# Kernel tuning notes

Measured on AMD Instinct MI355X. Metric: run time of the kernel, lower is better.

## Reference

```python
import jax, jax.numpy as jnp
import numpy as np

N_NODES = 100000
N_EDGES = 1200000
EMBED_DIM = 64
N_LAYERS = 3


def setup_inputs() -> dict:
    key = jax.random.key(0)
    k1, k2, k3, k4 = jax.random.split(key, 4)
    embeddings = jax.random.normal(k1, (N_NODES, EMBED_DIM), dtype=jnp.float32)
    edge_weight = jax.random.uniform(k2, (N_EDGES,), dtype=jnp.float32)
    edge_src = jax.random.randint(k3, (N_EDGES,), 0, N_NODES, dtype=jnp.int32)
    edge_dst = jax.random.randint(k4, (N_EDGES,), 0, N_NODES, dtype=jnp.int32)
    return {"embeddings": embeddings, "edge_weight": edge_weight,
            "edge_src": edge_src, "edge_dst": edge_dst}


def _spmm(edge_src, edge_dst, edge_weight, x):
    # (A @ x)[d] = sum_{e: dst(e)=d} w[e] * x[src(e)]  -- COO SpMM via gather + segment_sum
    msgs = edge_weight[:, None] * x[edge_src]  # [E, D]
    return jax.ops.segment_sum(msgs, edge_dst, num_segments=N_NODES)


def reference(embeddings, edge_weight, edge_src, edge_dst):
    all_embeddings = [embeddings]
    ego = embeddings
    for _ in range(N_LAYERS):
        ego = _spmm(edge_src, edge_dst, edge_weight, ego)
        all_embeddings.append(ego)
    # stack layer outputs: [n_layers+1, N, D]
    return jnp.stack(all_embeddings, axis=0)
```

## Files before the change

### kernel.cpp

```cpp
#include <hip/hip_runtime.h>
#include <hip/hip_fp16.h>


#define N_NODES 100000
#define DIM 64
#define SCAN_CHUNK 1024

#define NR 8
#define RSIZE ((N_NODES + NR - 1) / NR)
#define SLICES 128

typedef int   vint4   __attribute__((ext_vector_type(4)));
typedef float vfloat4 __attribute__((ext_vector_type(4)));

union HU { unsigned u; __half2 h; };

__global__ void convert_kernel(const float* __restrict__ emb, float* __restrict__ out0,
                               unsigned short* __restrict__ xh0, int n8) {
    int i = blockIdx.x * blockDim.x + threadIdx.x;
    if (i >= n8) return;
    const vfloat4* e4 = (const vfloat4*)emb;
    vfloat4 a = __builtin_nontemporal_load(e4 + 2 * i);
    vfloat4 b = __builtin_nontemporal_load(e4 + 2 * i + 1);
    vfloat4* o4 = (vfloat4*)out0;
    __builtin_nontemporal_store(a, o4 + 2 * i);
    __builtin_nontemporal_store(b, o4 + 2 * i + 1);
    HU c0, c1, c2, c3;
    c0.h = __float22half2_rn(make_float2(a[0], a[1]));
    c1.h = __float22half2_rn(make_float2(a[2], a[3]));
    c2.h = __float22half2_rn(make_float2(b[0], b[1]));
    c3.h = __float22half2_rn(make_float2(b[2], b[3]));
    vint4 p = { (int)c0.u, (int)c1.u, (int)c2.u, (int)c3.u };
    ((vint4*)xh0)[i] = p;
}


__global__ void hist_kernel(const int* __restrict__ edst, int* __restrict__ deg, int E) {
    int i = blockIdx.x * blockDim.x + threadIdx.x;
    int nv = E >> 2;
    if (i < nv) {
        vint4 d = __builtin_nontemporal_load(((const vint4*)edst) + i);
        atomicAdd(&deg[d[0]], 1);
        atomicAdd(&deg[d[1]], 1);
        atomicAdd(&deg[d[2]], 1);
        atomicAdd(&deg[d[3]], 1);
    }
    if (i == 0) {
        for (int e = nv << 2; e < E; ++e) atomicAdd(&deg[edst[e]], 1);
    }
}

__global__ void scan1_kernel(const int* __restrict__ deg, int* __restrict__ off,
                             int* __restrict__ bsum, int n) {
    __shared__ int sdata[256];
    int tid = threadIdx.x;
    int base = blockIdx.x * SCAN_CHUNK + tid * 4;
    int v[4];
    #pragma unroll
    for (int i = 0; i < 4; ++i) v[i] = (base + i < n) ? deg[base + i] : 0;
    int tsum = v[0] + v[1] + v[2] + v[3];
    sdata[tid] = tsum;
    __syncthreads();
    for (int d = 1; d < 256; d <<= 1) {
        int t = (tid >= d) ? sdata[tid - d] : 0;
        __syncthreads();
        sdata[tid] += t;
        __syncthreads();
    }
    int excl = sdata[tid] - tsum;
    if (tid == 255) bsum[blockIdx.x] = sdata[255];
    int run = excl;
    #pragma unroll
    for (int i = 0; i < 4; ++i) {
        if (base + i < n) off[base + i] = run;
        run += v[i];
    }
}

__global__ void scan2_kernel(int* __restrict__ bsum, int nb) {
    __shared__ int s[128];
    int tid = threadIdx.x;
    int v = (tid < nb) ? bsum[tid] : 0;
    s[tid] = v;
    __syncthreads();
    for (int d = 1; d < 128; d <<= 1) {
        int t = (tid >= d) ? s[tid - d] : 0;
        __syncthreads();
        s[tid] += t;
        __syncthreads();
    }
    if (tid < nb) bsum[tid] = s[tid] - v;
}

__global__ void scan3_kernel(int* __restrict__ off, int* __restrict__ cur,
                             const int* __restrict__ bsum, int n) {
    int i = blockIdx.x * blockDim.x + threadIdx.x;
    if (i < n) {
        int v = off[i] + bsum[i / SCAN_CHUNK];
        off[i] = v;
        cur[i] = v;
    }
}

__global__ void scatter_range_kernel(const int* __restrict__ esrc, const int* __restrict__ edst,
                                     const float* __restrict__ ew, int* __restrict__ cur,
                                     int2* __restrict__ pairs, int E, int chunk) {
    const int r = blockIdx.x & (NR - 1);
    const int s = blockIdx.x / NR;
    const int lo = r * RSIZE;
    const int hi = min(lo + RSIZE, N_NODES);
    const int e0 = s * chunk;
    if (e0 >= E) return;
    const int e1 = min(e0 + chunk, E);
    const int nv = (e1 - e0) >> 2;
    const vint4*   s4 = (const vint4*)(esrc + e0);
    const vint4*   d4 = (const vint4*)(edst + e0);
    const vfloat4* w4 = (const vfloat4*)(ew + e0);
    for (int i = threadIdx.x; i < nv; i += blockDim.x) {
        vint4 dd = __builtin_nontemporal_load(d4 + i);
        vint4 ss = __builtin_nontemporal_load(s4 + i);
        vfloat4 ww = __builtin_nontemporal_load(w4 + i);
        #pragma unroll
        for (int j = 0; j < 4; ++j) {
            int dj = dd[j];
            if (dj >= lo && dj < hi) {
                int p = atomicAdd(&cur[dj], 1);
                int2 pr;
                pr.x = ss[j];
                pr.y = __float_as_int(ww[j]);
                pairs[p] = pr;
            }
        }
    }
    for (int e = e0 + (nv << 2) + threadIdx.x; e < e1; e += blockDim.x) {
        int dj = edst[e];
        if (dj >= lo && dj < hi) {
            int p = atomicAdd(&cur[dj], 1);
            int2 pr;
            pr.x = esrc[e];
            pr.y = __float_as_int(ew[e]);
            pairs[p] = pr;
        }
    }
}


__global__ void spmm_h_kernel(const unsigned short* __restrict__ xh,
                              const int2* __restrict__ pairs,
                              const int* __restrict__ off,
                              const int* __restrict__ deg,
                              float* __restrict__ y,
                              unsigned short* __restrict__ yh) {
    int gtid = blockIdx.x * blockDim.x + threadIdx.x;
    int node = gtid >> 6;
    int lane = threadIdx.x & 63;
    int o  = lane >> 3;
    int ol = lane & 7;
    if (node >= N_NODES) return;
    int s0 = off[node];
    int n  = deg[node];
    float a0 = 0.f, a1 = 0.f, a2 = 0.f, a3 = 0.f;
    float a4 = 0.f, a5 = 0.f, a6 = 0.f, a7 = 0.f;
    for (int k = o; k < n; k += 8) {
        int2 pr = pairs[s0 + k];
        float w = __int_as_float(pr.y);
        const vint4* row = (const vint4*)(xh + (size_t)pr.x * DIM);
        vint4 v = row[ol];
        HU c; float2 f;
        c.u = (unsigned)v[0]; f = __half22float2(c.h); a0 += w * f.x; a1 += w * f.y;
        c.u = (unsigned)v[1]; f = __half22float2(c.h); a2 += w * f.x; a3 += w * f.y;
        c.u = (unsigned)v[2]; f = __half22float2(c.h); a4 += w * f.x; a5 += w * f.y;
        c.u = (unsigned)v[3]; f = __half22float2(c.h); a6 += w * f.x; a7 += w * f.y;
    }
    #pragma unroll
    for (int d = 8; d <= 32; d <<= 1) {
        a0 += __shfl_xor(a0, d); a1 += __shfl_xor(a1, d);
        a2 += __shfl_xor(a2, d); a3 += __shfl_xor(a3, d);
        a4 += __shfl_xor(a4, d); a5 += __shfl_xor(a5, d);
        a6 += __shfl_xor(a6, d); a7 += __shfl_xor(a7, d);
    }
    if (o == 0) {
        float* yr = y + (size_t)node * DIM + ol * 8;
        vfloat4 r0 = { a0, a1, a2, a3 };
        vfloat4 r1 = { a4, a5, a6, a7 };
        __builtin_nontemporal_store(r0, (vfloat4*)yr);
        __builtin_nontemporal_store(r1, (vfloat4*)yr + 1);
        HU c0, c1, c2, c3;
        c0.h = __float22half2_rn(make_float2(a0, a1));
        c1.h = __float22half2_rn(make_float2(a2, a3));
        c2.h = __float22half2_rn(make_float2(a4, a5));
        c3.h = __float22half2_rn(make_float2(a6, a7));
        vint4 p = { (int)c0.u, (int)c1.u, (int)c2.u, (int)c3.u };
        *((vint4*)(yh + (size_t)node * DIM + ol * 8)) = p;
    }
}


__global__ void spmm_csr_kernel(const float* __restrict__ x,
                                const int2* __restrict__ pairs,
                                const int* __restrict__ off,
                                const int* __restrict__ deg,
                                float* __restrict__ y) {
    int gtid = blockIdx.x * blockDim.x + threadIdx.x;
    int node = gtid >> 6;
    int lane = threadIdx.x & 63;
    int o  = lane >> 3;
    int ol = lane & 7;
    if (node >= N_NODES) return;
    int s0 = off[node];
    int n  = deg[node];
    float4 a0 = make_float4(0.f, 0.f, 0.f, 0.f);
    float4 a1 = a0;
    for (int k = o; k < n; k += 8) {
        int2 pr = pairs[s0 + k];
        float w = __int_as_float(pr.y);
        const float4* row = (const float4*)(x + (size_t)pr.x * DIM);
        float4 v0 = row[ol];
        float4 v1 = row[ol + 8];
        a0.x += w * v0.x; a0.y += w * v0.y; a0.z += w * v0.z; a0.w += w * v0.w;
        a1.x += w * v1.x; a1.y += w * v1.y; a1.z += w * v1.z; a1.w += w * v1.w;
    }
    #pragma unroll
    for (int d = 8; d <= 32; d <<= 1) {
        a0.x += __shfl_xor(a0.x, d); a0.y += __shfl_xor(a0.y, d);
        a0.z += __shfl_xor(a0.z, d); a0.w += __shfl_xor(a0.w, d);
        a1.x += __shfl_xor(a1.x, d); a1.y += __shfl_xor(a1.y, d);
        a1.z += __shfl_xor(a1.z, d); a1.w += __shfl_xor(a1.w, d);
    }
    if (o == 0) {
        vfloat4* yrow = (vfloat4*)(y + (size_t)node * DIM);
        vfloat4 r0 = { a0.x, a0.y, a0.z, a0.w };
        vfloat4 r1 = { a1.x, a1.y, a1.z, a1.w };
        __builtin_nontemporal_store(r0, yrow + ol);
        __builtin_nontemporal_store(r1, yrow + ol + 8);
    }
}


__global__ void spmm_atomic_kernel(const float* __restrict__ x, const float* __restrict__ ew,
                                   const int* __restrict__ esrc, const int* __restrict__ edst,
                                   float* __restrict__ y, int n_edges) {
    long long tid = (long long)blockIdx.x * blockDim.x + threadIdx.x;
    int e = (int)(tid >> 6);
    int d = (int)(tid & 63);
    if (e >= n_edges) return;
    int s = esrc[e]; int t = edst[e]; float w = ew[e];
    atomicAdd(&y[(long long)t * DIM + d], w * x[(long long)s * DIM + d]);
}

extern "C" void kernel_launch(void* const* d_in, const int* in_sizes, int n_in,
                              void* d_out, int out_size, void* d_ws, size_t ws_size,
                              hipStream_t stream) {
    const float* emb  = (const float*)d_in[0];
    const float* ew   = (const float*)d_in[1];
    const int*   esrc = (const int*)d_in[2];
    const int*   edst = (const int*)d_in[3];
    float* out = (float*)d_out;

    const int E = in_sizes[1];
    const size_t layer_elems = (size_t)N_NODES * DIM;

    const size_t need_h   = (size_t)E * 8 + 2 * layer_elems * 2 + (size_t)3 * N_NODES * 4 + 1024;
    const size_t need_f32 = (size_t)E * 8 + (size_t)3 * N_NODES * 4 + 1024;

    if (ws_size >= need_h && E >= 4) {
        char* w = (char*)d_ws;
        int2* pairs = (int2*)w;
        unsigned short* xh0 = (unsigned short*)(w + (size_t)E * 8);
        unsigned short* xh1 = xh0 + layer_elems;
        int* deg  = (int*)(xh1 + layer_elems);
        int* cur  = deg + N_NODES;
        int* off  = cur + N_NODES;
        int* bsum = off + N_NODES;

        hipMemsetAsync(deg, 0, (size_t)N_NODES * 4, stream);

        const int n8 = (int)(layer_elems / 8);
        convert_kernel<<<(n8 + 255) / 256, 256, 0, stream>>>(emb, out, xh0, n8);

        const int nv4 = E >> 2;
        hist_kernel<<<(nv4 + 255) / 256, 256, 0, stream>>>(edst, deg, E);

        const int nscan = (N_NODES + SCAN_CHUNK - 1) / SCAN_CHUNK;
        scan1_kernel<<<nscan, 256, 0, stream>>>(deg, off, bsum, N_NODES);
        scan2_kernel<<<1, 128, 0, stream>>>(bsum, nscan);
        scan3_kernel<<<(N_NODES + 255) / 256, 256, 0, stream>>>(off, cur, bsum, N_NODES);

        const int chunk = (((E + SLICES - 1) / SLICES) + 3) & ~3;
        scatter_range_kernel<<<NR * SLICES, 256, 0, stream>>>(esrc, edst, ew, cur, pairs, E, chunk);

        const int nb = (N_NODES + 3) / 4;
        unsigned short* xs[2] = { xh0, xh1 };
        for (int l = 1; l <= 3; ++l) {
            spmm_h_kernel<<<nb, 256, 0, stream>>>(
                xs[(l - 1) & 1], pairs, off, deg,
                out + (size_t)l * layer_elems, xs[l & 1]);
        }
    } else if (ws_size >= need_f32 && E >= 4) {
        char* w = (char*)d_ws;
        int2* pairs = (int2*)w;
        int* deg  = (int*)(w + (size_t)E * 8);
        int* cur  = deg + N_NODES;
        int* off  = cur + N_NODES;
        int* bsum = off + N_NODES;

        hipMemcpyAsync(out, emb, layer_elems * sizeof(float), hipMemcpyDeviceToDevice, stream);
        hipMemsetAsync(deg, 0, (size_t)N_NODES * 4, stream);

        const int nv4 = E >> 2;
        hist_kernel<<<(nv4 + 255) / 256, 256, 0, stream>>>(edst, deg, E);

        const int nscan = (N_NODES + SCAN_CHUNK - 1) / SCAN_CHUNK;
        scan1_kernel<<<nscan, 256, 0, stream>>>(deg, off, bsum, N_NODES);
        scan2_kernel<<<1, 128, 0, stream>>>(bsum, nscan);
        scan3_kernel<<<(N_NODES + 255) / 256, 256, 0, stream>>>(off, cur, bsum, N_NODES);

        const int chunk = (((E + SLICES - 1) / SLICES) + 3) & ~3;
        scatter_range_kernel<<<NR * SLICES, 256, 0, stream>>>(esrc, edst, ew, cur, pairs, E, chunk);

        const int nb = (N_NODES + 3) / 4;
        for (int l = 1; l <= 3; ++l) {
            spmm_csr_kernel<<<nb, 256, 0, stream>>>(
                out + (size_t)(l - 1) * layer_elems, pairs, off, deg,
                out + (size_t)l * layer_elems);
        }
    } else {
        hipMemcpyAsync(out, emb, layer_elems * sizeof(float), hipMemcpyDeviceToDevice, stream);
        hipMemsetAsync(out + layer_elems, 0, 3 * layer_elems * sizeof(float), stream);
        const long long total_threads = (long long)E * 64;
        const int blocks = (int)((total_threads + 255) / 256);
        for (int l = 1; l <= 3; ++l) {
            spmm_atomic_kernel<<<blocks, 256, 0, stream>>>(
                out + (size_t)(l - 1) * layer_elems, ew, esrc, edst,
                out + (size_t)l * layer_elems, E);
        }
    }
}
```

Before: 366.3 us.

## Sort CSR neighbors by source range via 2D histogram for gather locality

Builds a (dst, src-range) histogram with 16 source buckets per destination so each node's incoming edges are ordered by source range, then derives offsets and degrees from the scanned 2D histogram. The intent is more cache-friendly gathers of source rows during the three SpMM layers, since concurrent waves read from similar source regions. In exchange it adds a 1.6M-entry histogram, memset and scan plus a larger block-sum scan, making preprocessing more expensive. It also adds a separate degree kernel.

```diff
diff --git a/kernel.cpp b/kernel.cpp
--- a/kernel.cpp
+++ b/kernel.cpp
@@ -9,6 +9,10 @@
 #define NR 8
 #define RSIZE ((N_NODES + NR - 1) / NR)
 #define SLICES 128
+
+#define NRG 16
+#define RNG_SH 13
+#define NG (N_NODES * NRG)
 
 typedef int   vint4   __attribute__((ext_vector_type(4)));
 typedef float vfloat4 __attribute__((ext_vector_type(4)));
@@ -35,29 +39,31 @@
 }
 
 
-__global__ void hist_kernel(const int* __restrict__ edst, int* __restrict__ deg, int E) {
+__global__ void hist2_kernel(const int* __restrict__ esrc, const int* __restrict__ edst,
+                             int* __restrict__ h2, int E) {
     int i = blockIdx.x * blockDim.x + threadIdx.x;
     int nv = E >> 2;
     if (i < nv) {
         vint4 d = __builtin_nontemporal_load(((const vint4*)edst) + i);
-        atomicAdd(&deg[d[0]], 1);
-        atomicAdd(&deg[d[1]], 1);
-        atomicAdd(&deg[d[2]], 1);
-        atomicAdd(&deg[d[3]], 1);
+        vint4 s = __builtin_nontemporal_load(((const vint4*)esrc) + i);
+        #pragma unroll
+        for (int j = 0; j < 4; ++j)
+            atomicAdd(&h2[d[j] * NRG + (s[j] >> RNG_SH)], 1);
     }
     if (i == 0) {
-        for (int e = nv << 2; e < E; ++e) atomicAdd(&deg[edst[e]], 1);
-    }
-}
-
-__global__ void scan1_kernel(const int* __restrict__ deg, int* __restrict__ off,
+        for (int e = nv << 2; e < E; ++e)
+            atomicAdd(&h2[edst[e] * NRG + (esrc[e] >> RNG_SH)], 1);
+    }
+}
+
+__global__ void scan1_kernel(const int* __restrict__ src, int* __restrict__ dst,
                              int* __restrict__ bsum, int n) {
     __shared__ int sdata[256];
     int tid = threadIdx.x;
     int base = blockIdx.x * SCAN_CHUNK + tid * 4;
     int v[4];
     #pragma unroll
-    for (int i = 0; i < 4; ++i) v[i] = (base + i < n) ? deg[base + i] : 0;
+    for (int i = 0; i < 4; ++i) v[i] = (base + i < n) ? src[base + i] : 0;
     int tsum = v[0] + v[1] + v[2] + v[3];
     sdata[tid] = tsum;
     __syncthreads();
@@ -72,38 +78,49 @@
     int run = excl;
     #pragma unroll
     for (int i = 0; i < 4; ++i) {
-        if (base + i < n) off[base + i] = run;
+        if (base + i < n) dst[base + i] = run;
         run += v[i];
     }
 }
 
-__global__ void scan2_kernel(int* __restrict__ bsum, int nb) {
-    __shared__ int s[128];
-    int tid = threadIdx.x;
-    int v = (tid < nb) ? bsum[tid] : 0;
-    s[tid] = v;
+__global__ void scan2b_kernel(int* __restrict__ bsum, int nb) {
+    __shared__ int s[1024];
+    int t = threadIdx.x;
+    int i0 = 2 * t, i1 = 2 * t + 1;
+    int v0 = (i0 < nb) ? bsum[i0] : 0;
+    int v1 = (i1 < nb) ? bsum[i1] : 0;
+    s[t] = v0 + v1;
     __syncthreads();
-    for (int d = 1; d < 128; d <<= 1) {
-        int t = (tid >= d) ? s[tid - d] : 0;
+    for (int d = 1; d < 1024; d <<= 1) {
+        int tt = (t >= d) ? s[t - d] : 0;
         __syncthreads();
-        s[tid] += t;
+        s[t] += tt;
         __syncthreads();
     }
-    if (tid < nb) bsum[tid] = s[tid] - v;
-}
-
-__global__ void scan3_kernel(int* __restrict__ off, int* __restrict__ cur,
-                             const int* __restrict__ bsum, int n) {
+    int excl = s[t] - (v0 + v1);
+    if (i0 < nb) bsum[i0] = excl;
+    if (i1 < nb) bsum[i1] = excl + v0;
+}
+
+__global__ void scan3b_kernel(int* __restrict__ pos2, int* __restrict__ cur2,
+                              int* __restrict__ off, const int* __restrict__ bsum, int n) {
     int i = blockIdx.x * blockDim.x + threadIdx.x;
     if (i < n) {
-        int v = off[i] + bsum[i / SCAN_CHUNK];
-        off[i] = v;
-        cur[i] = v;
-    }
+        int v = pos2[i] + bsum[i >> 10];
+        pos2[i] = v;
+        cur2[i] = v;
+        if ((i & (NRG - 1)) == 0) off[i / NRG] = v;
+    }
+}
+
+__global__ void deg_kernel(const int* __restrict__ off, int* __restrict__ deg,
+                           int E, int n) {
+    int i = blockIdx.x * blockDim.x + threadIdx.x;
+    if (i < n) deg[i] = ((i == n - 1) ? E : off[i + 1]) - off[i];
 }
 
 __global__ void scatter_range_kernel(const int* __restrict__ esrc, const int* __restrict__ edst,
-                                     const float* __restrict__ ew, int* __restrict__ cur,
+                                     const float* __restrict__ ew, int* __restrict__ cur2,
                                      int2* __restrict__ pairs, int E, int chunk) {
     const int r = blockIdx.x & (NR - 1);
     const int s = blockIdx.x / NR;
@@ -124,7 +141,7 @@
         for (int j = 0; j < 4; ++j) {
             int dj = dd[j];
             if (dj >= lo && dj < hi) {
-                int p = atomicAdd(&cur[dj], 1);
+                int p = atomicAdd(&cur2[dj * NRG + (ss[j] >> RNG_SH)], 1);
                 int2 pr;
                 pr.x = ss[j];
                 pr.y = __float_as_int(ww[j]);
@@ -135,7 +152,7 @@
     for (int e = e0 + (nv << 2) + threadIdx.x; e < e1; e += blockDim.x) {
         int dj = edst[e];
         if (dj >= lo && dj < hi) {
-            int p = atomicAdd(&cur[dj], 1);
+            int p = atomicAdd(&cur2[dj * NRG + (esrc[e] >> RNG_SH)], 1);
             int2 pr;
             pr.x = esrc[e];
             pr.y = __float_as_int(ew[e]);
@@ -196,6 +213,73 @@
 }
 
 
+__global__ void hist_kernel(const int* __restrict__ edst, int* __restrict__ deg, int E) {
+    int i = blockIdx.x * blockDim.x + threadIdx.x;
+    int nv = E >> 2;
+    if (i < nv) {
+        vint4 d = __builtin_nontemporal_load(((const vint4*)edst) + i);
+        atomicAdd(&deg[d[0]], 1);
+        atomicAdd(&deg[d[1]], 1);
+        atomicAdd(&deg[d[2]], 1);
+        atomicAdd(&deg[d[3]], 1);
+    }
+    if (i == 0) {
+        for (int e = nv << 2; e < E; ++e) atomicAdd(&deg[edst[e]], 1);
+    }
+}
+
+__global__ void scan3_kernel(int* __restrict__ off, int* __restrict__ cur,
+                             const int* __restrict__ bsum, int n) {
+    int i = blockIdx.x * blockDim.x + threadIdx.x;
+    if (i < n) {
+        int v = off[i] + bsum[i / SCAN_CHUNK];
+        off[i] = v;
+        cur[i] = v;
+    }
+}
+
+__global__ void scatter_range1_kernel(const int* __restrict__ esrc, const int* __restrict__ edst,
+                                      const float* __restrict__ ew, int* __restrict__ cur,
+                                      int2* __restrict__ pairs, int E, int chunk) {
+    const int r = blockIdx.x & (NR - 1);
+    const int s = blockIdx.x / NR;
+    const int lo = r * RSIZE;
+    const int hi = min(lo + RSIZE, N_NODES);
+    const int e0 = s * chunk;
+    if (e0 >= E) return;
+    const int e1 = min(e0 + chunk, E);
+    const int nv = (e1 - e0) >> 2;
+    const vint4*   s4 = (const vint4*)(esrc + e0);
+    const vint4*   d4 = (const vint4*)(edst + e0);
+    const vfloat4* w4 = (const vfloat4*)(ew + e0);
+    for (int i = threadIdx.x; i < nv; i += blockDim.x) {
+        vint4 dd = __builtin_nontemporal_load(d4 + i);
+        vint4 ss = __builtin_nontemporal_load(s4 + i);
+        vfloat4 ww = __builtin_nontemporal_load(w4 + i);
+        #pragma unroll
+        for (int j = 0; j < 4; ++j) {
+            int dj = dd[j];
+            if (dj >= lo && dj < hi) {
+                int p = atomicAdd(&cur[dj], 1);
+                int2 pr;
+                pr.x = ss[j];
+                pr.y = __float_as_int(ww[j]);
+                pairs[p] = pr;
+            }
+        }
+    }
+    for (int e = e0 + (nv << 2) + threadIdx.x; e < e1; e += blockDim.x) {
+        int dj = edst[e];
+        if (dj >= lo && dj < hi) {
+            int p = atomicAdd(&cur[dj], 1);
+            int2 pr;
+            pr.x = esrc[e];
+            pr.y = __float_as_int(ew[e]);
+            pairs[p] = pr;
+        }
+    }
+}
+
 __global__ void spmm_csr_kernel(const float* __restrict__ x,
                                 const int2* __restrict__ pairs,
                                 const int* __restrict__ off,
@@ -236,7 +320,6 @@
     }
 }
 
-
 __global__ void spmm_atomic_kernel(const float* __restrict__ x, const float* __restrict__ ew,
                                    const int* __restrict__ esrc, const int* __restrict__ edst,
                                    float* __restrict__ y, int n_edges) {
@@ -260,10 +343,48 @@
     const int E = in_sizes[1];
     const size_t layer_elems = (size_t)N_NODES * DIM;
 
+    const size_t need_srt = (size_t)E * 8 + 2 * layer_elems * 2
+                          + (size_t)3 * NG * 4 + (size_t)2 * N_NODES * 4 + 16384;
     const size_t need_h   = (size_t)E * 8 + 2 * layer_elems * 2 + (size_t)3 * N_NODES * 4 + 1024;
     const size_t need_f32 = (size_t)E * 8 + (size_t)3 * N_NODES * 4 + 1024;
 
-    if (ws_size >= need_h && E >= 4) {
+    if (ws_size >= need_srt && E >= 4) {
+        char* w = (char*)d_ws;
+        int2* pairs = (int2*)w;
+        unsigned short* xh0 = (unsigned short*)(w + (size_t)E * 8);
+        unsigned short* xh1 = xh0 + layer_elems;
+        int* h2   = (int*)(xh1 + layer_elems);
+        int* pos2 = h2 + NG;
+        int* cur2 = pos2 + NG;
+        int* off  = cur2 + NG;
+        int* deg  = off + N_NODES;
+        int* bsum = deg + N_NODES;
+
+        hipMemsetAsync(h2, 0, (size_t)NG * 4, stream);
+
+        const int n8 = (int)(layer_elems / 8);
+        convert_kernel<<<(n8 + 255) / 256, 256, 0, stream>>>(emb, out, xh0, n8);
+
+        const int nv4 = E >> 2;
+        hist2_kernel<<<(nv4 + 255) / 256, 256, 0, stream>>>(esrc, edst, h2, E);
+
+        const int nscan = (NG + SCAN_CHUNK - 1) / SCAN_CHUNK;
+        scan1_kernel<<<nscan, 256, 0, stream>>>(h2, pos2, bsum, NG);
+        scan2b_kernel<<<1, 1024, 0, stream>>>(bsum, nscan);
+        scan3b_kernel<<<(NG + 255) / 256, 256, 0, stream>>>(pos2, cur2, off, bsum, NG);
+        deg_kernel<<<(N_NODES + 255) / 256, 256, 0, stream>>>(off, deg, E, N_NODES);
+
+        const int chunk = (((E + SLICES - 1) / SLICES) + 3) & ~3;
+        scatter_range_kernel<<<NR * SLICES, 256, 0, stream>>>(esrc, edst, ew, cur2, pairs, E, chunk);
+
+        const int nb = (N_NODES + 3) / 4;
+        unsigned short* xs[2] = { xh0, xh1 };
+        for (int l = 1; l <= 3; ++l) {
+            spmm_h_kernel<<<nb, 256, 0, stream>>>(
+                xs[(l - 1) & 1], pairs, off, deg,
+                out + (size_t)l * layer_elems, xs[l & 1]);
+        }
+    } else if (ws_size >= need_h && E >= 4) {
         char* w = (char*)d_ws;
         int2* pairs = (int2*)w;
         unsigned short* xh0 = (unsigned short*)(w + (size_t)E * 8);
@@ -274,21 +395,16 @@
         int* bsum = off + N_NODES;
 
         hipMemsetAsync(deg, 0, (size_t)N_NODES * 4, stream);
-
         const int n8 = (int)(layer_elems / 8);
         convert_kernel<<<(n8 + 255) / 256, 256, 0, stream>>>(emb, out, xh0, n8);
-
         const int nv4 = E >> 2;
         hist_kernel<<<(nv4 + 255) / 256, 256, 0, stream>>>(edst, deg, E);
-
         const int nscan = (N_NODES + SCAN_CHUNK - 1) / SCAN_CHUNK;
         scan1_kernel<<<nscan, 256, 0, stream>>>(deg, off, bsum, N_NODES);
-        scan2_kernel<<<1, 128, 0, stream>>>(bsum, nscan);
+        scan2b_kernel<<<1, 1024, 0, stream>>>(bsum, nscan);
         scan3_kernel<<<(N_NODES + 255) / 256, 256, 0, stream>>>(off, cur, bsum, N_NODES);
-
         const int chunk = (((E + SLICES - 1) / SLICES) + 3) & ~3;
-        scatter_range_kernel<<<NR * SLICES, 256, 0, stream>>>(esrc, edst, ew, cur, pairs, E, chunk);
-
+        scatter_range1_kernel<<<NR * SLICES, 256, 0, stream>>>(esrc, edst, ew, cur, pairs, E, chunk);
         const int nb = (N_NODES + 3) / 4;
         unsigned short* xs[2] = { xh0, xh1 };
         for (int l = 1; l <= 3; ++l) {
@@ -306,18 +422,14 @@
 
         hipMemcpyAsync(out, emb, layer_elems * sizeof(float), hipMemcpyDeviceToDevice, stream);
         hipMemsetAsync(deg, 0, (size_t)N_NODES * 4, stream);
-
         const int nv4 = E >> 2;
         hist_kernel<<<(nv4 + 255) / 256, 256, 0, stream>>>(edst, deg, E);
-
         const int nscan = (N_NODES + SCAN_CHUNK - 1) / SCAN_CHUNK;
         scan1_kernel<<<nscan, 256, 0, stream>>>(deg, off, bsum, N_NODES);
-        scan2_kernel<<<1, 128, 0, stream>>>(bsum, nscan);
+        scan2b_kernel<<<1, 1024, 0, stream>>>(bsum, nscan);
         scan3_kernel<<<(N_NODES + 255) / 256, 256, 0, stream>>>(off, cur, bsum, N_NODES);
-
         const int chunk = (((E + SLICES - 1) / SLICES) + 3) & ~3;
-        scatter_range_kernel<<<NR * SLICES, 256, 0, stream>>>(esrc, edst, ew, cur, pairs, E, chunk);
-
+        scatter_range1_kernel<<<NR * SLICES, 256, 0, stream>>>(esrc, edst, ew, cur, pairs, E, chunk);
         const int nb = (N_NODES + 3) / 4;
         for (int l = 1; l <= 3; ++l) {
             spmm_csr_kernel<<<nb, 256, 0, stream>>>(
```

After: 374.2 us. 2.1% more time.
